# Performance work log

Measured on AMD Instinct MI355X. Metric: run time of the kernel, lower is better.

Reference implementation:

```python
import jax, jax.numpy as jnp
import numpy as np


def setup_inputs() -> dict:
    key = jax.random.key(0)
    ks = jax.random.split(key, 6)
    B, C, H, W = 8, 128, 64, 64
    return {
        "curr_features": jax.random.normal(ks[0], (B, C, H, W), jnp.float32),
        "w1": jax.random.normal(ks[1], (C, 2 * C), jnp.float32) * 0.05,   # conv1x1 (2C->C)
        "b1": jnp.zeros((C,), jnp.float32),
        "gamma": jnp.ones((C,), jnp.float32),
        "beta": jnp.zeros((C,), jnp.float32),
        "running_mean": jax.random.normal(ks[2], (C,), jnp.float32) * 0.1,
        "running_var": jax.random.uniform(ks[3], (C,), jnp.float32, 0.5, 1.5),
        "w2": jax.random.normal(ks[4], (1, C), jnp.float32) * 0.05,       # conv1x1 (C->1)
        "b2": jnp.zeros((1,), jnp.float32),
    }


def reference(curr_features, w1, b1, gamma, beta, running_mean, running_var, w2, b2):
    B, C, H, W = curr_features.shape
    M = H * W
    BN_EPS = 1e-5
    LEAKY_SLOPE = 0.01  # InPlaceABNSync default activation: leaky_relu(0.01)

    f = curr_features.reshape(B, C, M)                       # [B,C,M]
    scores = jnp.einsum('bcm,bcn->bmn', f, f) * (C ** -0.5)  # [B,M,M]
    p = jax.nn.softmax(scores, axis=-1)
    feats1 = jnp.einsum('bmn,bcn->bcm', p, f)                # [B,C,M]

    x = jnp.concatenate([feats1, f], axis=1).reshape(B, 2 * C, H, W)

    # cls head: conv1x1 -> BN(inference) -> leaky_relu -> (dropout=identity in eval) -> conv1x1
    y = jnp.einsum('oc,bchw->bohw', w1, x) + b1[None, :, None, None]
    scale = gamma / jnp.sqrt(running_var + BN_EPS)
    y = (y - running_mean[None, :, None, None]) * scale[None, :, None, None] + beta[None, :, None, None]
    y = jnp.where(y >= 0, y, LEAKY_SLOPE * y)
    pred = jnp.einsum('oc,bchw->bohw', w2, y) + b2[None, :, None, None]  # [B,1,H,W]
    return pred
```

## Files before the change

### kernel.cpp

```cpp
#include <hip/hip_runtime.h>

#define NB 8
#define NC 128
#define NM 4096
#define FRAG 512

typedef __attribute__((ext_vector_type(8))) short short8;
typedef __attribute__((ext_vector_type(4))) float floatx4;

#define MFMA(a, b, c) __builtin_amdgcn_mfma_f32_16x16x32_bf16(a, b, c, 0, 0, 0)
#define EXP2F(x) __builtin_amdgcn_exp2f(x)

union S8U { short8 v; uint2 u2[2]; };

__device__ __forceinline__ unsigned pack2bf(float a, float b) {
    unsigned ua = __float_as_uint(a);
    unsigned ub = __float_as_uint(b);
    ua += 0x7fffu + ((ua >> 16) & 1u);
    ub += 0x7fffu + ((ub >> 16) & 1u);
    return (ua >> 16) | (ub & 0xffff0000u);
}

__device__ __forceinline__ unsigned cvt_pk_bf16(float a, float b) {
    unsigned r;
    asm("v_cvt_pk_bf16_f32 %0, %1, %2" : "=v"(r) : "v"(a), "v"(b));
    return r;
}

__constant__ float SF_C = 0.35712442f;
__constant__ float RS_C = 2.8001530f;


__global__ __launch_bounds__(256) void k_prep_f(
    const float* __restrict__ f, unsigned short* __restrict__ fX)
{
    __shared__ float Ls[128][65];
    const int tid = threadIdx.x;
    const int b   = blockIdx.x & 7;
    const int m0  = (blockIdx.x >> 3) * 64;
    const float* fb = f + (size_t)b * NC * NM;
    #pragma unroll
    for (int k = 0; k < 32; ++k) {
        int idx = tid + k * 256;
        int c = idx >> 6, mm = idx & 63;
        Ls[c][mm] = fb[(size_t)c * NM + m0 + mm];
    }
    __syncthreads();
    const float sf = SF_C;
    const int m  = tid >> 2;
    const int ks = tid & 3;
    const int ch = ks * 32;
    unsigned pk[16];
    #pragma unroll
    for (int i = 0; i < 16; ++i)
        pk[i] = pack2bf(Ls[ch + 2 * i][m] * sf, Ls[ch + 2 * i + 1][m] * sf);
    const int Mg  = m0 + m;
    const int mt  = Mg >> 4;
    const int lmm = Mg & 15;
    unsigned short* dst = fX + ((size_t)b * 256 + mt) * 4 * FRAG + ks * FRAG;
    #pragma unroll
    for (int q = 0; q < 4; ++q)
        *(uint4*)(dst + (q * 16 + lmm) * 8) =
            make_uint4(pk[4 * q], pk[4 * q + 1], pk[4 * q + 2], pk[4 * q + 3]);
}

__global__ __launch_bounds__(256) void k_prep_g(
    const unsigned short* __restrict__ fX, const float* __restrict__ w1,
    unsigned short* __restrict__ gX)
{
    __shared__ unsigned short gt[128][136];
    const int tid = threadIdx.x;
    const int wv  = tid >> 6;
    const int l   = tid & 63;
    const int lm  = l & 15;
    const int lq  = l >> 4;
    const int b    = blockIdx.x & 7;
    const int nblk = blockIdx.x >> 3;

    const float rs = RS_C;

    short8 wf2[2][4];
    #pragma unroll
    for (int j = 0; j < 2; ++j) {
        const int o = (wv * 2 + j) * 16 + lm;
        #pragma unroll
        for (int ks = 0; ks < 4; ++ks) {
            const float* wp = w1 + (size_t)o * (2 * NC) + ks * 32 + lq * 8;
            S8U t;
            t.u2[0] = make_uint2(pack2bf(wp[0] * rs, wp[1] * rs),
                                 pack2bf(wp[2] * rs, wp[3] * rs));
            t.u2[1] = make_uint2(pack2bf(wp[4] * rs, wp[5] * rs),
                                 pack2bf(wp[6] * rs, wp[7] * rs));
            wf2[j][ks] = t.v;
        }
    }

    const unsigned short* fXb = fX + (size_t)b * NM * NC;
    #pragma unroll 2
    for (int nt = 0; nt < 8; ++nt) {
        short8 af[4];
        #pragma unroll
        for (int ks = 0; ks < 4; ++ks)
            af[ks] = *(const short8*)
                (fXb + (size_t)(nblk * 8 + nt) * 4 * FRAG + ks * FRAG + l * 8);
        #pragma unroll
        for (int j = 0; j < 2; ++j) {
            floatx4 D = {0.f, 0.f, 0.f, 0.f};
            #pragma unroll
            for (int ks = 0; ks < 4; ++ks)
                D = MFMA(af[ks], wf2[j][ks], D);
            *(uint2*)&gt[(wv * 2 + j) * 16 + lm][nt * 16 + lq * 4] =
                make_uint2(pack2bf(D[0], D[1]), pack2bf(D[2], D[3]));
        }
    }
    __syncthreads();

    #pragma unroll
    for (int j = 0; j < 2; ++j) {
        const int ot = wv * 2 + j;
        #pragma unroll
        for (int k2 = 0; k2 < 4; ++k2) {
            uint4 v = *(const uint4*)&gt[ot * 16 + lm][k2 * 32 + lq * 8];
            *(uint4*)(gX + (((size_t)b * 32 + nblk) * 8 + ot) * 4 * FRAG
                      + k2 * FRAG + l * 8) = v;
        }
    }
}

__global__ __launch_bounds__(256, 2) void k_attn(
    const unsigned short* __restrict__ fX,
    const unsigned short* __restrict__ gX,
    const float* __restrict__ w1,
    const float* __restrict__ b1v, const float* __restrict__ gammav,
    const float* __restrict__ betav, const float* __restrict__ rmeanv,
    const float* __restrict__ rvarv, const float* __restrict__ w2v,
    const float* __restrict__ b2v, float* __restrict__ out)
{
    __shared__ __align__(16) char Ps[2][16384];
    __shared__ float lpart[4][64];
    __shared__ float opart[4][64];

    const int tid = threadIdx.x;
    const int w   = tid >> 6;
    const int l   = tid & 63;
    const int lm  = l & 15;
    const int lq  = l >> 4;
    const int b   = blockIdx.x & 7;
    const int m0  = (blockIdx.x >> 3) * 64;

    const int lq0 = lq & 1;
    const int lq1 = lq >> 1;
    const int lm3 = lm >> 3;
    const unsigned Xsw = (unsigned)(((lq1 << 1) | lm3) << 4);
    const unsigned wofsA =
        ((((unsigned)(w >> 1) * 4 * 16) + ((unsigned)(2 * (w & 1) + lq1) * 16)
          + (unsigned)lm) * 16 + (unsigned)(8 * lq0)) ^ Xsw;
    const unsigned rofs = ((unsigned)l * 16) ^ ((((unsigned)l >> 3) & 3u) << 4);

    const unsigned short* fXb = fX + (size_t)b * NM * NC;
    const unsigned short* gXb = gX + (size_t)b * NC * NM;

    short8 qf[4][4];
    {
        const int qt0 = m0 >> 4;
        #pragma unroll
        for (int mt = 0; mt < 4; ++mt)
            #pragma unroll
            for (int ks = 0; ks < 4; ++ks)
                qf[mt][ks] = *(const short8*)
                    (fXb + (size_t)(qt0 + mt) * 4 * FRAG + ks * FRAG + l * 8);
    }

    const unsigned short* kpA = fXb + (size_t)w * 4 * FRAG + l * 8;
    const unsigned short* kpB = fXb + (size_t)(4 + w) * 4 * FRAG + l * 8;
    const unsigned short* gp0 = gXb + (size_t)(2 * w) * 4 * FRAG + l * 8;
    const unsigned short* gp1 = gXb + (size_t)(2 * w + 1) * 4 * FRAG + l * 8;

    short8 kfA[4], kfB[4], gf0[4], gf1[4];
    #pragma unroll
    for (int ks = 0; ks < 4; ++ks) {
        kfA[ks] = *(const short8*)(kpA + ks * FRAG);
        kfB[ks] = *(const short8*)(kpB + ks * FRAG);
    }
    #pragma unroll
    for (int k2 = 0; k2 < 4; ++k2) {
        gf0[k2] = *(const short8*)(gp0 + k2 * FRAG);
        gf1[k2] = *(const short8*)(gp1 + k2 * FRAG);
    }

    floatx4 u[4][2];
    float lsum[4] = {0.f, 0.f, 0.f, 0.f};
    #pragma unroll
    for (int mt = 0; mt < 4; ++mt) {
        u[mt][0] = (floatx4){0.f, 0.f, 0.f, 0.f};
        u[mt][1] = (floatx4){0.f, 0.f, 0.f, 0.f};
    }

    for (int it = 0; it < 32; ++it) {
        const int buf = it & 1;
        char* psb = Ps[buf];

        floatx4 svA[4], svB[4];
        __builtin_amdgcn_s_setprio(1);
        #pragma unroll
        for (int mt = 0; mt < 4; ++mt) {
            floatx4 a = {-24.f, -24.f, -24.f, -24.f};
            floatx4 bb = {-24.f, -24.f, -24.f, -24.f};
            #pragma unroll
            for (int ks = 0; ks < 4; ++ks) {
                a  = MFMA(kfA[ks], qf[mt][ks], a);
                bb = MFMA(kfB[ks], qf[mt][ks], bb);
            }
            svA[mt] = a; svB[mt] = bb;
        }
        __builtin_amdgcn_s_setprio(0);
        {
            const int kstep = (it < 31) ? 8 * 4 * FRAG : 0;
            kpA += kstep; kpB += kstep;
            #pragma unroll
            for (int ks = 0; ks < 4; ++ks) {
                kfA[ks] = *(const short8*)(kpA + ks * FRAG);
                kfB[ks] = *(const short8*)(kpB + ks * FRAG);
            }
        }

        #pragma unroll
        for (int mt = 0; mt < 4; ++mt) {
            float pA0 = EXP2F(svA[mt][0]);
            float pA1 = EXP2F(svA[mt][1]);
            float pA2 = EXP2F(svA[mt][2]);
            float pA3 = EXP2F(svA[mt][3]);
            float pB0 = EXP2F(svB[mt][0]);
            float pB1 = EXP2F(svB[mt][1]);
            float pB2 = EXP2F(svB[mt][2]);
            float pB3 = EXP2F(svB[mt][3]);
            lsum[mt] += ((pA0 + pA1) + (pA2 + pA3)) +
                        ((pB0 + pB1) + (pB2 + pB3));
            *(uint2*)(psb + mt * 4096 + wofsA) =
                make_uint2(cvt_pk_bf16(pA0, pA1), cvt_pk_bf16(pA2, pA3));
            *(uint2*)(psb + mt * 4096 + wofsA + 2048) =
                make_uint2(cvt_pk_bf16(pB0, pB1), cvt_pk_bf16(pB2, pB3));
        }
        __syncthreads();

        #pragma unroll
        for (int k2 = 0; k2 < 4; ++k2) {
            short8 pf[4];
            #pragma unroll
            for (int mt = 0; mt < 4; ++mt)
                pf[mt] = *(const short8*)(psb + mt * 4096 + k2 * 1024 + rofs);
            __builtin_amdgcn_s_setprio(1);
            #pragma unroll
            for (int mt = 0; mt < 4; ++mt) {
                u[mt][0] = MFMA(pf[mt], gf0[k2], u[mt][0]);
                u[mt][1] = MFMA(pf[mt], gf1[k2], u[mt][1]);
            }
            __builtin_amdgcn_s_setprio(0);
        }
        {
            const int gstep = (it < 31) ? 8 * 4 * FRAG : 0;
            gp0 += gstep; gp1 += gstep;
            #pragma unroll
            for (int k2 = 0; k2 < 4; ++k2) {
                gf0[k2] = *(const short8*)(gp0 + k2 * FRAG);
                gf1[k2] = *(const short8*)(gp1 + k2 * FRAG);
            }
        }
    }

    #pragma unroll
    for (int mt = 0; mt < 4; ++mt) {
        lsum[mt] += __shfl_xor(lsum[mt], 16);
        lsum[mt] += __shfl_xor(lsum[mt], 32);
    }
    if (lq == 0) {
        #pragma unroll
        for (int mt = 0; mt < 4; ++mt)
            lpart[w][mt * 16 + lm] = lsum[mt];
    }

    floatx4 hacc[4][2];
    {
        const float rs = RS_C;
        #pragma unroll
        for (int j = 0; j < 2; ++j) {
            int o = w * 32 + j * 16 + lm;
            short8 wf[4];
            #pragma unroll
            for (int ks = 0; ks < 4; ++ks) {
                const float* wp = w1 + (size_t)o * (2 * NC) + NC + ks * 32 + lq * 8;
                S8U t;
                t.u2[0] = make_uint2(pack2bf(wp[0] * rs, wp[1] * rs),
                                     pack2bf(wp[2] * rs, wp[3] * rs));
                t.u2[1] = make_uint2(pack2bf(wp[4] * rs, wp[5] * rs),
                                     pack2bf(wp[6] * rs, wp[7] * rs));
                wf[ks] = t.v;
            }
            #pragma unroll
            for (int mt = 0; mt < 4; ++mt) {
                floatx4 a = {0.f, 0.f, 0.f, 0.f};
                #pragma unroll
                for (int ks = 0; ks < 4; ++ks)
                    a = MFMA(qf[mt][ks], wf[ks], a);
                hacc[mt][j] = a;
            }
        }
    }
    __syncthreads();

    float Abn[2], Dbn[2], W2[2];
    #pragma unroll
    for (int j = 0; j < 2; ++j) {
        int o = w * 32 + j * 16 + lm;
        float Ar = gammav[o] * rsqrtf(rvarv[o] + 1e-5f);
        Abn[j] = Ar;
        Dbn[j] = (b1v[o] - rmeanv[o]) * Ar + betav[o];
        W2[j]  = w2v[o];
    }
    float av[16];
    #pragma unroll
    for (int mt = 0; mt < 4; ++mt) {
        float4 L0 = *(const float4*)&lpart[0][mt * 16 + lq * 4];
        float4 L1 = *(const float4*)&lpart[1][mt * 16 + lq * 4];
        float4 L2 = *(const float4*)&lpart[2][mt * 16 + lq * 4];
        float4 L3 = *(const float4*)&lpart[3][mt * 16 + lq * 4];
        float4 Lt;
        Lt.x = (L0.x + L1.x) + (L2.x + L3.x);
        Lt.y = (L0.y + L1.y) + (L2.y + L3.y);
        Lt.z = (L0.z + L1.z) + (L2.z + L3.z);
        Lt.w = (L0.w + L1.w) + (L2.w + L3.w);
        #pragma unroll
        for (int r = 0; r < 4; ++r) {
            float rl = 1.f / ((const float*)&Lt)[r];
            float t0 = Abn[0] * (u[mt][0][r] * rl + hacc[mt][0][r]) + Dbn[0];
            float t1 = Abn[1] * (u[mt][1][r] * rl + hacc[mt][1][r]) + Dbn[1];
            t0 = t0 >= 0.f ? t0 : 0.01f * t0;
            t1 = t1 >= 0.f ? t1 : 0.01f * t1;
            av[mt * 4 + r] = W2[0] * t0 + W2[1] * t1;
        }
    }
    #pragma unroll
    for (int i = 0; i < 16; ++i) {
        av[i] += __shfl_xor(av[i], 1);
        av[i] += __shfl_xor(av[i], 2);
        av[i] += __shfl_xor(av[i], 4);
        av[i] += __shfl_xor(av[i], 8);
    }
    if (lm == 0) {
        #pragma unroll
        for (int mt = 0; mt < 4; ++mt)
            #pragma unroll
            for (int r = 0; r < 4; ++r)
                opart[w][mt * 16 + lq * 4 + r] = av[mt * 4 + r];
    }
    __syncthreads();
    if (tid < 64)
        out[(size_t)b * NM + m0 + tid] =
            b2v[0] + opart[0][tid] + opart[1][tid] + opart[2][tid] + opart[3][tid];
}

extern "C" void kernel_launch(void* const* d_in, const int* in_sizes, int n_in,
                              void* d_out, int out_size, void* d_ws, size_t ws_size,
                              hipStream_t stream) {
    const float* f     = (const float*)d_in[0];
    const float* w1    = (const float*)d_in[1];
    const float* b1    = (const float*)d_in[2];
    const float* gamma = (const float*)d_in[3];
    const float* beta  = (const float*)d_in[4];
    const float* rmean = (const float*)d_in[5];
    const float* rvar  = (const float*)d_in[6];
    const float* w2    = (const float*)d_in[7];
    const float* b2    = (const float*)d_in[8];
    float* out = (float*)d_out;

    unsigned short* fX = (unsigned short*)d_ws;
    unsigned short* gX = fX + (size_t)NB * NM * NC;

    hipLaunchKernelGGL(k_prep_f, dim3(512), dim3(256), 0, stream, f, fX);
    hipLaunchKernelGGL(k_prep_g, dim3(256), dim3(256), 0, stream, fX, w1, gX);
    hipLaunchKernelGGL(k_attn,   dim3(512), dim3(256), 0, stream,
                       fX, gX, w1, b1, gamma, beta, rmean, rvar, w2, b2, out);
}
```

Measured before the change: 156.9 us.

## Split attention key range across two wave groups per block with LDS reduction

The attention kernel now launches 512 threads per block. It is split into two groups of four waves, and each group processes half of the key/value sequence (16 iterations instead of 32) using its own P double-buffer in 64KB of shared memory. At the end, the second group dumps its partial output accumulators to LDS, the first group adds them, and softmax denominators are summed across all eight waves. This raises per-block wave parallelism and halves the serial loop length, at the cost of more LDS, an extra reduction step and tighter occupancy/register limits (launch_bounds 512,4).

```diff
diff --git a/kernel.cpp b/kernel.cpp
--- a/kernel.cpp
+++ b/kernel.cpp
@@ -127,7 +127,7 @@
     }
 }
 
-__global__ __launch_bounds__(256, 2) void k_attn(
+__global__ __launch_bounds__(512, 4) void k_attn(
     const unsigned short* __restrict__ fX,
     const unsigned short* __restrict__ gX,
     const float* __restrict__ w1,
@@ -136,24 +136,26 @@
     const float* __restrict__ rvarv, const float* __restrict__ w2v,
     const float* __restrict__ b2v, float* __restrict__ out)
 {
-    __shared__ __align__(16) char Ps[2][16384];
-    __shared__ float lpart[4][64];
-    __shared__ float opart[4][64];
+    __shared__ __align__(16) char smem[65536];
 
     const int tid = threadIdx.x;
     const int w   = tid >> 6;
+    const int g   = w >> 2;
+    const int wg  = w & 3;
     const int l   = tid & 63;
     const int lm  = l & 15;
     const int lq  = l >> 4;
     const int b   = blockIdx.x & 7;
     const int m0  = (blockIdx.x >> 3) * 64;
 
+    char* ps_g = smem + g * 32768;
+
     const int lq0 = lq & 1;
     const int lq1 = lq >> 1;
     const int lm3 = lm >> 3;
     const unsigned Xsw = (unsigned)(((lq1 << 1) | lm3) << 4);
     const unsigned wofsA =
-        ((((unsigned)(w >> 1) * 4 * 16) + ((unsigned)(2 * (w & 1) + lq1) * 16)
+        ((((unsigned)(wg >> 1) * 4 * 16) + ((unsigned)(2 * (wg & 1) + lq1) * 16)
           + (unsigned)lm) * 16 + (unsigned)(8 * lq0)) ^ Xsw;
     const unsigned rofs = ((unsigned)l * 16) ^ ((((unsigned)l >> 3) & 3u) << 4);
 
@@ -171,10 +173,10 @@
                     (fXb + (size_t)(qt0 + mt) * 4 * FRAG + ks * FRAG + l * 8);
     }
 
-    const unsigned short* kpA = fXb + (size_t)w * 4 * FRAG + l * 8;
-    const unsigned short* kpB = fXb + (size_t)(4 + w) * 4 * FRAG + l * 8;
-    const unsigned short* gp0 = gXb + (size_t)(2 * w) * 4 * FRAG + l * 8;
-    const unsigned short* gp1 = gXb + (size_t)(2 * w + 1) * 4 * FRAG + l * 8;
+    const unsigned short* kpA = fXb + (size_t)(g * 128 + wg) * 4 * FRAG + l * 8;
+    const unsigned short* kpB = fXb + (size_t)(g * 128 + 4 + wg) * 4 * FRAG + l * 8;
+    const unsigned short* gp0 = gXb + (size_t)(g * 128 + 2 * wg) * 4 * FRAG + l * 8;
+    const unsigned short* gp1 = gXb + (size_t)(g * 128 + 2 * wg + 1) * 4 * FRAG + l * 8;
 
     short8 kfA[4], kfB[4], gf0[4], gf1[4];
     #pragma unroll
@@ -196,9 +198,8 @@
         u[mt][1] = (floatx4){0.f, 0.f, 0.f, 0.f};
     }
 
-    for (int it = 0; it < 32; ++it) {
-        const int buf = it & 1;
-        char* psb = Ps[buf];
+    for (int it = 0; it < 16; ++it) {
+        char* psb = ps_g + (it & 1) * 16384;
 
         floatx4 svA[4], svB[4];
         __builtin_amdgcn_s_setprio(1);
@@ -215,7 +216,7 @@
         }
         __builtin_amdgcn_s_setprio(0);
         {
-            const int kstep = (it < 31) ? 8 * 4 * FRAG : 0;
+            const int kstep = (it < 15) ? 8 * 4 * FRAG : 0;
             kpA += kstep; kpB += kstep;
             #pragma unroll
             for (int ks = 0; ks < 4; ++ks) {
@@ -258,7 +259,7 @@
             __builtin_amdgcn_s_setprio(0);
         }
         {
-            const int gstep = (it < 31) ? 8 * 4 * FRAG : 0;
+            const int gstep = (it < 15) ? 8 * 4 * FRAG : 0;
             gp0 += gstep; gp1 += gstep;
             #pragma unroll
             for (int k2 = 0; k2 < 4; ++k2) {
@@ -268,6 +269,10 @@
         }
     }
 
+    float* lpartf = (float*)smem;
+    float* opartf = (float*)(smem + 2048);
+    float* udump  = (float*)(smem + 32768);
+
     #pragma unroll
     for (int mt = 0; mt < 4; ++mt) {
         lsum[mt] += __shfl_xor(lsum[mt], 16);
@@ -276,87 +281,106 @@
     if (lq == 0) {
         #pragma unroll
         for (int mt = 0; mt < 4; ++mt)
-            lpart[w][mt * 16 + lm] = lsum[mt];
-    }
-
-    floatx4 hacc[4][2];
-    {
-        const float rs = RS_C;
+            lpartf[w * 64 + mt * 16 + lm] = lsum[mt];
+    }
+    __syncthreads();
+
+    if (w >= 4) {
+        float* ud = udump + (size_t)wg * 2048 + l * 4;
+        #pragma unroll
+        for (int mt = 0; mt < 4; ++mt)
+            #pragma unroll
+            for (int j = 0; j < 2; ++j)
+                *(floatx4*)(ud + (mt * 2 + j) * 256) = u[mt][j];
+    }
+    __syncthreads();
+
+    if (w < 4) {
+        {
+            const float* ud = udump + (size_t)w * 2048 + l * 4;
+            #pragma unroll
+            for (int mt = 0; mt < 4; ++mt)
+                #pragma unroll
+                for (int j = 0; j < 2; ++j)
+                    u[mt][j] += *(const floatx4*)(ud + (mt * 2 + j) * 256);
+        }
+
+        floatx4 hacc[4][2];
+        {
+            const float rs = RS_C;
+            #pragma unroll
+            for (int j = 0; j < 2; ++j) {
+                int o = w * 32 + j * 16 + lm;
+                short8 wf[4];
+                #pragma unroll
+                for (int ks = 0; ks < 4; ++ks) {
+                    const float* wp = w1 + (size_t)o * (2 * NC) + NC + ks * 32 + lq * 8;
+                    S8U t;
+                    t.u2[0] = make_uint2(pack2bf(wp[0] * rs, wp[1] * rs),
+                                         pack2bf(wp[2] * rs, wp[3] * rs));
+                    t.u2[1] = make_uint2(pack2bf(wp[4] * rs, wp[5] * rs),
+                                         pack2bf(wp[6] * rs, wp[7] * rs));
+                    wf[ks] = t.v;
+                }
+                #pragma unroll
+                for (int mt = 0; mt < 4; ++mt) {
+                    floatx4 a = {0.f, 0.f, 0.f, 0.f};
+                    #pragma unroll
+                    for (int ks = 0; ks < 4; ++ks)
+                        a = MFMA(qf[mt][ks], wf[ks], a);
+                    hacc[mt][j] = a;
+                }
+            }
+        }
+
+        float Abn[2], Dbn[2], W2[2];
         #pragma unroll
         for (int j = 0; j < 2; ++j) {
             int o = w * 32 + j * 16 + lm;
-            short8 wf[4];
-            #pragma unroll
-            for (int ks = 0; ks < 4; ++ks) {
-                const float* wp = w1 + (size_t)o * (2 * NC) + NC + ks * 32 + lq * 8;
-                S8U t;
-                t.u2[0] = make_uint2(pack2bf(wp[0] * rs, wp[1] * rs),
-                                     pack2bf(wp[2] * rs, wp[3] * rs));
-                t.u2[1] = make_uint2(pack2bf(wp[4] * rs, wp[5] * rs),
-                                     pack2bf(wp[6] * rs, wp[7] * rs));
-                wf[ks] = t.v;
-            }
-            #pragma unroll
-            for (int mt = 0; mt < 4; ++mt) {
-                floatx4 a = {0.f, 0.f, 0.f, 0.f};
+            float Ar = gammav[o] * rsqrtf(rvarv[o] + 1e-5f);
+            Abn[j] = Ar;
+            Dbn[j] = (b1v[o] - rmeanv[o]) * Ar + betav[o];
+            W2[j]  = w2v[o];
+        }
+        float av[16];
+        #pragma unroll
+        for (int mt = 0; mt < 4; ++mt) {
+            float4 Lt = make_float4(0.f, 0.f, 0.f, 0.f);
+            #pragma unroll
+            for (int p = 0; p < 8; ++p) {
+                float4 Lp = *(const float4*)&lpartf[p * 64 + mt * 16 + lq * 4];
+                Lt.x += Lp.x; Lt.y += Lp.y; Lt.z += Lp.z; Lt.w += Lp.w;
+            }
+            #pragma unroll
+            for (int r = 0; r < 4; ++r) {
+                float rl = 1.f / ((const float*)&Lt)[r];
+                float t0 = Abn[0] * (u[mt][0][r] * rl + hacc[mt][0][r]) + Dbn[0];
+                float t1 = Abn[1] * (u[mt][1][r] * rl + hacc[mt][1][r]) + Dbn[1];
+                t0 = t0 >= 0.f ? t0 : 0.01f * t0;
+                t1 = t1 >= 0.f ? t1 : 0.01f * t1;
+                av[mt * 4 + r] = W2[0] * t0 + W2[1] * t1;
+            }
+        }
+        #pragma unroll
+        for (int i = 0; i < 16; ++i) {
+            av[i] += __shfl_xor(av[i], 1);
+            av[i] += __shfl_xor(av[i], 2);
+            av[i] += __shfl_xor(av[i], 4);
+            av[i] += __shfl_xor(av[i], 8);
+        }
+        if (lm == 0) {
+            #pragma unroll
+            for (int mt = 0; mt < 4; ++mt)
                 #pragma unroll
-                for (int ks = 0; ks < 4; ++ks)
-                    a = MFMA(qf[mt][ks], wf[ks], a);
-                hacc[mt][j] = a;
-            }
-        }
-    }
-    __syncthreads();
-
-    float Abn[2], Dbn[2], W2[2];
-    #pragma unroll
-    for (int j = 0; j < 2; ++j) {
-        int o = w * 32 + j * 16 + lm;
-        float Ar = gammav[o] * rsqrtf(rvarv[o] + 1e-5f);
-        Abn[j] = Ar;
-        Dbn[j] = (b1v[o] - rmeanv[o]) * Ar + betav[o];
-        W2[j]  = w2v[o];
-    }
-    float av[16];
-    #pragma unroll
-    for (int mt = 0; mt < 4; ++mt) {
-        float4 L0 = *(const float4*)&lpart[0][mt * 16 + lq * 4];
-        float4 L1 = *(const float4*)&lpart[1][mt * 16 + lq * 4];
-        float4 L2 = *(const float4*)&lpart[2][mt * 16 + lq * 4];
-        float4 L3 = *(const float4*)&lpart[3][mt * 16 + lq * 4];
-        float4 Lt;
-        Lt.x = (L0.x + L1.x) + (L2.x + L3.x);
-        Lt.y = (L0.y + L1.y) + (L2.y + L3.y);
-        Lt.z = (L0.z + L1.z) + (L2.z + L3.z);
-        Lt.w = (L0.w + L1.w) + (L2.w + L3.w);
-        #pragma unroll
-        for (int r = 0; r < 4; ++r) {
-            float rl = 1.f / ((const float*)&Lt)[r];
-            float t0 = Abn[0] * (u[mt][0][r] * rl + hacc[mt][0][r]) + Dbn[0];
-            float t1 = Abn[1] * (u[mt][1][r] * rl + hacc[mt][1][r]) + Dbn[1];
-            t0 = t0 >= 0.f ? t0 : 0.01f * t0;
-            t1 = t1 >= 0.f ? t1 : 0.01f * t1;
-            av[mt * 4 + r] = W2[0] * t0 + W2[1] * t1;
-        }
-    }
-    #pragma unroll
-    for (int i = 0; i < 16; ++i) {
-        av[i] += __shfl_xor(av[i], 1);
-        av[i] += __shfl_xor(av[i], 2);
-        av[i] += __shfl_xor(av[i], 4);
-        av[i] += __shfl_xor(av[i], 8);
-    }
-    if (lm == 0) {
-        #pragma unroll
-        for (int mt = 0; mt < 4; ++mt)
-            #pragma unroll
-            for (int r = 0; r < 4; ++r)
-                opart[w][mt * 16 + lq * 4 + r] = av[mt * 4 + r];
+                for (int r = 0; r < 4; ++r)
+                    opartf[w * 64 + mt * 16 + lq * 4 + r] = av[mt * 4 + r];
+        }
     }
     __syncthreads();
     if (tid < 64)
         out[(size_t)b * NM + m0 + tid] =
-            b2v[0] + opart[0][tid] + opart[1][tid] + opart[2][tid] + opart[3][tid];
+            b2v[0] + opartf[tid] + opartf[64 + tid] +
+            opartf[128 + tid] + opartf[192 + tid];
 }
 
 extern "C" void kernel_launch(void* const* d_in, const int* in_sizes, int n_in,
@@ -378,6 +402,6 @@
 
     hipLaunchKernelGGL(k_prep_f, dim3(512), dim3(256), 0, stream, f, fX);
     hipLaunchKernelGGL(k_prep_g, dim3(256), dim3(256), 0, stream, fX, w1, gX);
-    hipLaunchKernelGGL(k_attn,   dim3(512), dim3(256), 0, stream,
+    hipLaunchKernelGGL(k_attn,   dim3(512), dim3(512), 0, stream,
                        fX, gX, w1, b1, gamma, beta, rmean, rvar, w2, b2, out);
 }
```

Result: slower. 403.4 us (+157.1%).

## Halve attention query tile to 32 rows and double occupancy

Applied to the files above, without the earlier changes.

The attention kernel now handles 32 query rows per block instead of 64. Grid size doubles to 1024 blocks, launch bounds rise to 4 blocks per CU, and LDS shrinks to a single 8KB buffer. Each loop iteration now processes 64 keys instead of 128, over 64 iterations, with smaller register fragments and a new prefetch index for g. The aim is more waves per CU to hide latency and fill all CUs, at the cost of re-reading K and G twice as often per query and running more barriers.

```diff
diff --git a/kernel.cpp b/kernel.cpp
--- a/kernel.cpp
+++ b/kernel.cpp
@@ -127,7 +127,7 @@
     }
 }
 
-__global__ __launch_bounds__(256, 2) void k_attn(
+__global__ __launch_bounds__(256, 4) void k_attn(
     const unsigned short* __restrict__ fX,
     const unsigned short* __restrict__ gX,
     const float* __restrict__ w1,
@@ -136,9 +136,7 @@
     const float* __restrict__ rvarv, const float* __restrict__ w2v,
     const float* __restrict__ b2v, float* __restrict__ out)
 {
-    __shared__ __align__(16) char Ps[2][16384];
-    __shared__ float lpart[4][64];
-    __shared__ float opart[4][64];
+    __shared__ __align__(16) char smem[8192];
 
     const int tid = threadIdx.x;
     const int w   = tid >> 6;
@@ -146,140 +144,130 @@
     const int lm  = l & 15;
     const int lq  = l >> 4;
     const int b   = blockIdx.x & 7;
-    const int m0  = (blockIdx.x >> 3) * 64;
+    const int m0  = (blockIdx.x >> 3) * 32;
 
     const int lq0 = lq & 1;
     const int lq1 = lq >> 1;
     const int lm3 = lm >> 3;
     const unsigned Xsw = (unsigned)(((lq1 << 1) | lm3) << 4);
-    const unsigned wofsA =
-        ((((unsigned)(w >> 1) * 4 * 16) + ((unsigned)(2 * (w & 1) + lq1) * 16)
-          + (unsigned)lm) * 16 + (unsigned)(8 * lq0)) ^ Xsw;
+    const unsigned wofs =
+        ((unsigned)(w >> 1) * 1024 +
+         ((((unsigned)(2 * (w & 1) + lq1) * 16) + (unsigned)lm) * 16 +
+          (unsigned)(8 * lq0))) ^ Xsw;
     const unsigned rofs = ((unsigned)l * 16) ^ ((((unsigned)l >> 3) & 3u) << 4);
 
     const unsigned short* fXb = fX + (size_t)b * NM * NC;
     const unsigned short* gXb = gX + (size_t)b * NC * NM;
 
-    short8 qf[4][4];
+    short8 qf[2][4];
     {
         const int qt0 = m0 >> 4;
         #pragma unroll
-        for (int mt = 0; mt < 4; ++mt)
+        for (int mt = 0; mt < 2; ++mt)
             #pragma unroll
             for (int ks = 0; ks < 4; ++ks)
                 qf[mt][ks] = *(const short8*)
                     (fXb + (size_t)(qt0 + mt) * 4 * FRAG + ks * FRAG + l * 8);
     }
 
-    const unsigned short* kpA = fXb + (size_t)w * 4 * FRAG + l * 8;
-    const unsigned short* kpB = fXb + (size_t)(4 + w) * 4 * FRAG + l * 8;
-    const unsigned short* gp0 = gXb + (size_t)(2 * w) * 4 * FRAG + l * 8;
-    const unsigned short* gp1 = gXb + (size_t)(2 * w + 1) * 4 * FRAG + l * 8;
-
-    short8 kfA[4], kfB[4], gf0[4], gf1[4];
-    #pragma unroll
-    for (int ks = 0; ks < 4; ++ks) {
-        kfA[ks] = *(const short8*)(kpA + ks * FRAG);
-        kfB[ks] = *(const short8*)(kpB + ks * FRAG);
-    }
-    #pragma unroll
-    for (int k2 = 0; k2 < 4; ++k2) {
-        gf0[k2] = *(const short8*)(gp0 + k2 * FRAG);
-        gf1[k2] = *(const short8*)(gp1 + k2 * FRAG);
-    }
-
-    floatx4 u[4][2];
-    float lsum[4] = {0.f, 0.f, 0.f, 0.f};
-    #pragma unroll
-    for (int mt = 0; mt < 4; ++mt) {
+    const unsigned short* kp = fXb + (size_t)w * 4 * FRAG + l * 8;
+    short8 kf[4];
+    #pragma unroll
+    for (int ks = 0; ks < 4; ++ks)
+        kf[ks] = *(const short8*)(kp + ks * FRAG);
+
+    short8 gf[2][2];
+    #pragma unroll
+    for (int j = 0; j < 2; ++j)
+        #pragma unroll
+        for (int k2l = 0; k2l < 2; ++k2l)
+            gf[j][k2l] = *(const short8*)
+                (gXb + ((size_t)(2 * w + j) * 4 + k2l) * FRAG + l * 8);
+
+    floatx4 u[2][2];
+    float lsum[2] = {0.f, 0.f};
+    #pragma unroll
+    for (int mt = 0; mt < 2; ++mt) {
         u[mt][0] = (floatx4){0.f, 0.f, 0.f, 0.f};
         u[mt][1] = (floatx4){0.f, 0.f, 0.f, 0.f};
     }
 
-    for (int it = 0; it < 32; ++it) {
-        const int buf = it & 1;
-        char* psb = Ps[buf];
-
-        floatx4 svA[4], svB[4];
+    for (int it = 0; it < 64; ++it) {
+        char* psb = smem + (it & 1) * 4096;
+
+        floatx4 sv[2];
         __builtin_amdgcn_s_setprio(1);
         #pragma unroll
-        for (int mt = 0; mt < 4; ++mt) {
+        for (int mt = 0; mt < 2; ++mt) {
             floatx4 a = {-24.f, -24.f, -24.f, -24.f};
-            floatx4 bb = {-24.f, -24.f, -24.f, -24.f};
-            #pragma unroll
-            for (int ks = 0; ks < 4; ++ks) {
-                a  = MFMA(kfA[ks], qf[mt][ks], a);
-                bb = MFMA(kfB[ks], qf[mt][ks], bb);
-            }
-            svA[mt] = a; svB[mt] = bb;
+            #pragma unroll
+            for (int ks = 0; ks < 4; ++ks)
+                a = MFMA(kf[ks], qf[mt][ks], a);
+            sv[mt] = a;
         }
         __builtin_amdgcn_s_setprio(0);
         {
-            const int kstep = (it < 31) ? 8 * 4 * FRAG : 0;
-            kpA += kstep; kpB += kstep;
-            #pragma unroll
-            for (int ks = 0; ks < 4; ++ks) {
-                kfA[ks] = *(const short8*)(kpA + ks * FRAG);
-                kfB[ks] = *(const short8*)(kpB + ks * FRAG);
-            }
-        }
-
-        #pragma unroll
-        for (int mt = 0; mt < 4; ++mt) {
-            float pA0 = EXP2F(svA[mt][0]);
-            float pA1 = EXP2F(svA[mt][1]);
-            float pA2 = EXP2F(svA[mt][2]);
-            float pA3 = EXP2F(svA[mt][3]);
-            float pB0 = EXP2F(svB[mt][0]);
-            float pB1 = EXP2F(svB[mt][1]);
-            float pB2 = EXP2F(svB[mt][2]);
-            float pB3 = EXP2F(svB[mt][3]);
-            lsum[mt] += ((pA0 + pA1) + (pA2 + pA3)) +
-                        ((pB0 + pB1) + (pB2 + pB3));
-            *(uint2*)(psb + mt * 4096 + wofsA) =
-                make_uint2(cvt_pk_bf16(pA0, pA1), cvt_pk_bf16(pA2, pA3));
-            *(uint2*)(psb + mt * 4096 + wofsA + 2048) =
-                make_uint2(cvt_pk_bf16(pB0, pB1), cvt_pk_bf16(pB2, pB3));
+            const int kstep = (it < 63) ? 16 * FRAG : 0;
+            kp += kstep;
+            #pragma unroll
+            for (int ks = 0; ks < 4; ++ks)
+                kf[ks] = *(const short8*)(kp + ks * FRAG);
+        }
+
+        #pragma unroll
+        for (int mt = 0; mt < 2; ++mt) {
+            float p0 = EXP2F(sv[mt][0]);
+            float p1 = EXP2F(sv[mt][1]);
+            float p2 = EXP2F(sv[mt][2]);
+            float p3 = EXP2F(sv[mt][3]);
+            lsum[mt] += (p0 + p1) + (p2 + p3);
+            *(uint2*)(psb + mt * 2048 + wofs) =
+                make_uint2(cvt_pk_bf16(p0, p1), cvt_pk_bf16(p2, p3));
         }
         __syncthreads();
 
         #pragma unroll
-        for (int k2 = 0; k2 < 4; ++k2) {
-            short8 pf[4];
-            #pragma unroll
-            for (int mt = 0; mt < 4; ++mt)
-                pf[mt] = *(const short8*)(psb + mt * 4096 + k2 * 1024 + rofs);
+        for (int k2l = 0; k2l < 2; ++k2l) {
+            short8 pf[2];
+            #pragma unroll
+            for (int mt = 0; mt < 2; ++mt)
+                pf[mt] = *(const short8*)(psb + mt * 2048 + k2l * 1024 + rofs);
             __builtin_amdgcn_s_setprio(1);
             #pragma unroll
-            for (int mt = 0; mt < 4; ++mt) {
-                u[mt][0] = MFMA(pf[mt], gf0[k2], u[mt][0]);
-                u[mt][1] = MFMA(pf[mt], gf1[k2], u[mt][1]);
+            for (int mt = 0; mt < 2; ++mt) {
+                u[mt][0] = MFMA(pf[mt], gf[0][k2l], u[mt][0]);
+                u[mt][1] = MFMA(pf[mt], gf[1][k2l], u[mt][1]);
             }
             __builtin_amdgcn_s_setprio(0);
         }
-        {
-            const int gstep = (it < 31) ? 8 * 4 * FRAG : 0;
-            gp0 += gstep; gp1 += gstep;
-            #pragma unroll
-            for (int k2 = 0; k2 < 4; ++k2) {
-                gf0[k2] = *(const short8*)(gp0 + k2 * FRAG);
-                gf1[k2] = *(const short8*)(gp1 + k2 * FRAG);
-            }
-        }
-    }
-
-    #pragma unroll
-    for (int mt = 0; mt < 4; ++mt) {
+        if (it < 63) {
+            const int nit = it + 1;
+            const unsigned short* gb = gXb +
+                ((size_t)(nit >> 1) * 32 + (size_t)(2 * w) * 4 +
+                 (size_t)(nit & 1) * 2) * FRAG + l * 8;
+            #pragma unroll
+            for (int j = 0; j < 2; ++j)
+                #pragma unroll
+                for (int k2l = 0; k2l < 2; ++k2l)
+                    gf[j][k2l] = *(const short8*)(gb + (j * 4 + k2l) * FRAG);
+        }
+    }
+
+    float* lpartf = (float*)smem;
+    float* opartf = (float*)(smem + 512);
+
+    #pragma unroll
+    for (int mt = 0; mt < 2; ++mt) {
         lsum[mt] += __shfl_xor(lsum[mt], 16);
         lsum[mt] += __shfl_xor(lsum[mt], 32);
     }
     if (lq == 0) {
         #pragma unroll
-        for (int mt = 0; mt < 4; ++mt)
-            lpart[w][mt * 16 + lm] = lsum[mt];
-    }
-
-    floatx4 hacc[4][2];
+        for (int mt = 0; mt < 2; ++mt)
+            lpartf[w * 32 + mt * 16 + lm] = lsum[mt];
+    }
+
+    floatx4 hacc[2][2];
     {
         const float rs = RS_C;
         #pragma unroll
@@ -297,7 +285,7 @@
                 wf[ks] = t.v;
             }
             #pragma unroll
-            for (int mt = 0; mt < 4; ++mt) {
+            for (int mt = 0; mt < 2; ++mt) {
                 floatx4 a = {0.f, 0.f, 0.f, 0.f};
                 #pragma unroll
                 for (int ks = 0; ks < 4; ++ks)
@@ -317,13 +305,13 @@
         Dbn[j] = (b1v[o] - rmeanv[o]) * Ar + betav[o];
         W2[j]  = w2v[o];
     }
-    float av[16];
-    #pragma unroll
-    for (int mt = 0; mt < 4; ++mt) {
-        float4 L0 = *(const float4*)&lpart[0][mt * 16 + lq * 4];
-        float4 L1 = *(const float4*)&lpart[1][mt * 16 + lq * 4];
-        float4 L2 = *(const float4*)&lpart[2][mt * 16 + lq * 4];
-        float4 L3 = *(const float4*)&lpart[3][mt * 16 + lq * 4];
+    float av[8];
+    #pragma unroll
+    for (int mt = 0; mt < 2; ++mt) {
+        float4 L0 = *(const float4*)&lpartf[0 * 32 + mt * 16 + lq * 4];
+        float4 L1 = *(const float4*)&lpartf[1 * 32 + mt * 16 + lq * 4];
+        float4 L2 = *(const float4*)&lpartf[2 * 32 + mt * 16 + lq * 4];
+        float4 L3 = *(const float4*)&lpartf[3 * 32 + mt * 16 + lq * 4];
         float4 Lt;
         Lt.x = (L0.x + L1.x) + (L2.x + L3.x);
         Lt.y = (L0.y + L1.y) + (L2.y + L3.y);
@@ -340,7 +328,7 @@
         }
     }
     #pragma unroll
-    for (int i = 0; i < 16; ++i) {
+    for (int i = 0; i < 8; ++i) {
         av[i] += __shfl_xor(av[i], 1);
         av[i] += __shfl_xor(av[i], 2);
         av[i] += __shfl_xor(av[i], 4);
@@ -348,15 +336,16 @@
     }
     if (lm == 0) {
         #pragma unroll
-        for (int mt = 0; mt < 4; ++mt)
+        for (int mt = 0; mt < 2; ++mt)
             #pragma unroll
             for (int r = 0; r < 4; ++r)
-                opart[w][mt * 16 + lq * 4 + r] = av[mt * 4 + r];
+                opartf[w * 32 + mt * 16 + lq * 4 + r] = av[mt * 4 + r];
     }
     __syncthreads();
-    if (tid < 64)
+    if (tid < 32)
         out[(size_t)b * NM + m0 + tid] =
-            b2v[0] + opart[0][tid] + opart[1][tid] + opart[2][tid] + opart[3][tid];
+            b2v[0] + opartf[tid] + opartf[32 + tid] +
+            opartf[64 + tid] + opartf[96 + tid];
 }
 
 extern "C" void kernel_launch(void* const* d_in, const int* in_sizes, int n_in,
@@ -378,6 +367,6 @@
 
     hipLaunchKernelGGL(k_prep_f, dim3(512), dim3(256), 0, stream, f, fX);
     hipLaunchKernelGGL(k_prep_g, dim3(256), dim3(256), 0, stream, fX, w1, gX);
-    hipLaunchKernelGGL(k_attn,   dim3(512), dim3(256), 0, stream,
+    hipLaunchKernelGGL(k_attn,   dim3(1024), dim3(256), 0, stream,
                        fX, gX, w1, b1, gamma, beta, rmean, rvar, w2, b2, out);
 }
```

After: 177.0 us. 1.13x slower.

## Software-pipeline QK softmax ahead of PV with 4 LDS P buffers

Applied to the files above, without the earlier changes.

Restructures the attention loop so that the QK^T plus exp stage for tile i+2 runs alongside the P·V MFMA stage for tile i. P tiles cycle through four LDS buffers, which cuts the barrier count to one per two tiles, and two register sets of V fragments are double-buffered. The aim is to overlap exp and LDS-write latency with MFMA work and to remove half of the __syncthreads. In exchange, LDS use rises from 32KB to 64KB per block and register pressure goes up, which may lower occupancy under launch_bounds(256,2). The lpart/opart scratch arrays now alias the P buffer.

```diff
diff --git a/kernel.cpp b/kernel.cpp
--- a/kernel.cpp
+++ b/kernel.cpp
@@ -136,9 +136,7 @@
     const float* __restrict__ rvarv, const float* __restrict__ w2v,
     const float* __restrict__ b2v, float* __restrict__ out)
 {
-    __shared__ __align__(16) char Ps[2][16384];
-    __shared__ float lpart[4][64];
-    __shared__ float opart[4][64];
+    __shared__ __align__(16) char Ps[4][16384];
 
     const int tid = threadIdx.x;
     const int w   = tid >> 6;
@@ -176,7 +174,8 @@
     const unsigned short* gp0 = gXb + (size_t)(2 * w) * 4 * FRAG + l * 8;
     const unsigned short* gp1 = gXb + (size_t)(2 * w + 1) * 4 * FRAG + l * 8;
 
-    short8 kfA[4], kfB[4], gf0[4], gf1[4];
+    short8 kfA[4], kfB[4];
+    short8 gA0[4], gA1[4], gB0[4], gB1[4];
     #pragma unroll
     for (int ks = 0; ks < 4; ++ks) {
         kfA[ks] = *(const short8*)(kpA + ks * FRAG);
@@ -184,8 +183,14 @@
     }
     #pragma unroll
     for (int k2 = 0; k2 < 4; ++k2) {
-        gf0[k2] = *(const short8*)(gp0 + k2 * FRAG);
-        gf1[k2] = *(const short8*)(gp1 + k2 * FRAG);
+        gA0[k2] = *(const short8*)(gp0 + k2 * FRAG);
+        gA1[k2] = *(const short8*)(gp1 + k2 * FRAG);
+    }
+    gp0 += 8 * 4 * FRAG; gp1 += 8 * 4 * FRAG;
+    #pragma unroll
+    for (int k2 = 0; k2 < 4; ++k2) {
+        gB0[k2] = *(const short8*)(gp0 + k2 * FRAG);
+        gB1[k2] = *(const short8*)(gp1 + k2 * FRAG);
     }
 
     floatx4 u[4][2];
@@ -196,10 +201,7 @@
         u[mt][1] = (floatx4){0.f, 0.f, 0.f, 0.f};
     }
 
-    for (int it = 0; it < 32; ++it) {
-        const int buf = it & 1;
-        char* psb = Ps[buf];
-
+    auto qksm = [&](char* psW, bool loadK) {
         floatx4 svA[4], svB[4];
         __builtin_amdgcn_s_setprio(1);
         #pragma unroll
@@ -214,16 +216,14 @@
             svA[mt] = a; svB[mt] = bb;
         }
         __builtin_amdgcn_s_setprio(0);
-        {
-            const int kstep = (it < 31) ? 8 * 4 * FRAG : 0;
-            kpA += kstep; kpB += kstep;
+        if (loadK) {
+            kpA += 8 * 4 * FRAG; kpB += 8 * 4 * FRAG;
             #pragma unroll
             for (int ks = 0; ks < 4; ++ks) {
                 kfA[ks] = *(const short8*)(kpA + ks * FRAG);
                 kfB[ks] = *(const short8*)(kpB + ks * FRAG);
             }
         }
-
         #pragma unroll
         for (int mt = 0; mt < 4; ++mt) {
             float pA0 = EXP2F(svA[mt][0]);
@@ -236,37 +236,58 @@
             float pB3 = EXP2F(svB[mt][3]);
             lsum[mt] += ((pA0 + pA1) + (pA2 + pA3)) +
                         ((pB0 + pB1) + (pB2 + pB3));
-            *(uint2*)(psb + mt * 4096 + wofsA) =
+            *(uint2*)(psW + mt * 4096 + wofsA) =
                 make_uint2(cvt_pk_bf16(pA0, pA1), cvt_pk_bf16(pA2, pA3));
-            *(uint2*)(psb + mt * 4096 + wofsA + 2048) =
+            *(uint2*)(psW + mt * 4096 + wofsA + 2048) =
                 make_uint2(cvt_pk_bf16(pB0, pB1), cvt_pk_bf16(pB2, pB3));
         }
-        __syncthreads();
-
+    };
+    auto pv = [&](char* psR, short8 (&g0)[4], short8 (&g1)[4]) {
         #pragma unroll
         for (int k2 = 0; k2 < 4; ++k2) {
             short8 pf[4];
             #pragma unroll
             for (int mt = 0; mt < 4; ++mt)
-                pf[mt] = *(const short8*)(psb + mt * 4096 + k2 * 1024 + rofs);
+                pf[mt] = *(const short8*)(psR + mt * 4096 + k2 * 1024 + rofs);
             __builtin_amdgcn_s_setprio(1);
             #pragma unroll
             for (int mt = 0; mt < 4; ++mt) {
-                u[mt][0] = MFMA(pf[mt], gf0[k2], u[mt][0]);
-                u[mt][1] = MFMA(pf[mt], gf1[k2], u[mt][1]);
+                u[mt][0] = MFMA(pf[mt], g0[k2], u[mt][0]);
+                u[mt][1] = MFMA(pf[mt], g1[k2], u[mt][1]);
             }
             __builtin_amdgcn_s_setprio(0);
         }
-        {
-            const int gstep = (it < 31) ? 8 * 4 * FRAG : 0;
-            gp0 += gstep; gp1 += gstep;
-            #pragma unroll
-            for (int k2 = 0; k2 < 4; ++k2) {
-                gf0[k2] = *(const short8*)(gp0 + k2 * FRAG);
-                gf1[k2] = *(const short8*)(gp1 + k2 * FRAG);
-            }
-        }
-    }
+    };
+    auto gload = [&](short8 (&g0)[4], short8 (&g1)[4]) {
+        gp0 += 8 * 4 * FRAG; gp1 += 8 * 4 * FRAG;
+        #pragma unroll
+        for (int k2 = 0; k2 < 4; ++k2) {
+            g0[k2] = *(const short8*)(gp0 + k2 * FRAG);
+            g1[k2] = *(const short8*)(gp1 + k2 * FRAG);
+        }
+    };
+
+    qksm(Ps[0], true);
+    __syncthreads();
+    qksm(Ps[1], true);
+
+    for (int i = 0; i < 7; ++i) {
+        qksm(Ps[2], true); pv(Ps[0], gA0, gA1); gload(gA0, gA1);
+        __syncthreads();
+        qksm(Ps[3], true); pv(Ps[1], gB0, gB1); gload(gB0, gB1);
+        qksm(Ps[0], true); pv(Ps[2], gA0, gA1); gload(gA0, gA1);
+        __syncthreads();
+        qksm(Ps[1], true); pv(Ps[3], gB0, gB1); gload(gB0, gB1);
+    }
+    qksm(Ps[2], true); pv(Ps[0], gA0, gA1); gload(gA0, gA1);
+    __syncthreads();
+    qksm(Ps[3], false); pv(Ps[1], gB0, gB1); gload(gB0, gB1);
+    __syncthreads();
+    pv(Ps[2], gA0, gA1);
+    pv(Ps[3], gB0, gB1);
+
+    float* lpart = (float*)Ps;
+    float* opart = (float*)Ps + 256;
 
     #pragma unroll
     for (int mt = 0; mt < 4; ++mt) {
@@ -276,7 +297,7 @@
     if (lq == 0) {
         #pragma unroll
         for (int mt = 0; mt < 4; ++mt)
-            lpart[w][mt * 16 + lm] = lsum[mt];
+            lpart[w * 64 + mt * 16 + lm] = lsum[mt];
     }
 
     floatx4 hacc[4][2];
@@ -320,10 +341,10 @@
     float av[16];
     #pragma unroll
     for (int mt = 0; mt < 4; ++mt) {
-        float4 L0 = *(const float4*)&lpart[0][mt * 16 + lq * 4];
-        float4 L1 = *(const float4*)&lpart[1][mt * 16 + lq * 4];
-        float4 L2 = *(const float4*)&lpart[2][mt * 16 + lq * 4];
-        float4 L3 = *(const float4*)&lpart[3][mt * 16 + lq * 4];
+        float4 L0 = *(const float4*)&lpart[0 * 64 + mt * 16 + lq * 4];
+        float4 L1 = *(const float4*)&lpart[1 * 64 + mt * 16 + lq * 4];
+        float4 L2 = *(const float4*)&lpart[2 * 64 + mt * 16 + lq * 4];
+        float4 L3 = *(const float4*)&lpart[3 * 64 + mt * 16 + lq * 4];
         float4 Lt;
         Lt.x = (L0.x + L1.x) + (L2.x + L3.x);
         Lt.y = (L0.y + L1.y) + (L2.y + L3.y);
@@ -351,12 +372,13 @@
         for (int mt = 0; mt < 4; ++mt)
             #pragma unroll
             for (int r = 0; r < 4; ++r)
-                opart[w][mt * 16 + lq * 4 + r] = av[mt * 4 + r];
+                opart[w * 64 + mt * 16 + lq * 4 + r] = av[mt * 4 + r];
     }
     __syncthreads();
     if (tid < 64)
         out[(size_t)b * NM + m0 + tid] =
-            b2v[0] + opart[0][tid] + opart[1][tid] + opart[2][tid] + opart[3][tid];
+            b2v[0] + opart[tid] + opart[64 + tid] +
+            opart[128 + tid] + opart[192 + tid];
 }
 
 extern "C" void kernel_launch(void* const* d_in, const int* in_sizes, int n_in,
```

Measured after the change: 156.9 us. About the same (+0.0%).
